# Kernel tuning notes

Hardware: AMD Instinct MI355X
Metric: run time of the kernel (lower is better)

## Reference

```python
import jax, jax.numpy as jnp
import numpy as np

N_NODES = 100000
N_EDGES = 3200000
IN_FEATS = 16
OUT_FEATS = 2
K = 3


def setup_inputs() -> dict:
    key = jax.random.key(0)
    k1, k2, k3, k4 = jax.random.split(key, 4)
    in_feat = jax.random.normal(k1, (N_NODES, IN_FEATS), dtype=jnp.float32)
    # Linear(K*in_feats -> out_feats, bias=False) weight, torch layout (out, in)
    W = jax.random.normal(k2, (OUT_FEATS, K * IN_FEATS), dtype=jnp.float32) * (1.0 / np.sqrt(K * IN_FEATS))
    src = jax.random.randint(k3, (N_EDGES,), 0, N_NODES, dtype=jnp.int64)
    dst = jax.random.randint(k4, (N_EDGES,), 0, N_NODES, dtype=jnp.int64)
    # cached dgl.laplacian_lambda_max value; 2.0 is the normalized-Laplacian bound
    lambda_max = jnp.full((1,), 2.0, dtype=jnp.float32)
    return {"in_feat": in_feat, "W": W, "src": src, "dst": dst, "lambda_max": lambda_max}


def reference(in_feat, W, src, dst, lambda_max):
    N = in_feat.shape[0]
    # in-degree based symmetric normalization, clamp(min=1)
    deg = jax.ops.segment_sum(jnp.ones_like(dst, dtype=in_feat.dtype), dst, num_segments=N)
    norm = jnp.clip(deg, 1.0) ** -0.5  # (N,)
    norm = norm[:, None]
    re_norm = (2.0 / lambda_max)[None, :]  # (1,1), broadcasts over nodes

    def prop(x):
        # D^{-1/2} A D^{-1/2} x via gather from src, scatter-sum to dst
        m = (x * norm)[src]                                    # (E, d)
        return jax.ops.segment_sum(m, dst, num_segments=N) * norm

    X0 = in_feat
    X1 = -re_norm * prop(X0) + X0 * (re_norm - 1.0)
    X2 = -2.0 * re_norm * prop(X1) + X1 * (2.0 * (re_norm - 1.0)) - X0
    Xt = jnp.concatenate([X0, X1, X2], axis=1)                 # (N, K*d)
    h = Xt @ W.T                                               # (N, out)
    return jax.nn.relu(h)  # DGL ChebConv default activation
```

## Files before the change

kernel.cpp:

```cpp
#include <hip/hip_runtime.h>
#include <hip/hip_bf16.h>


#define NN   100000
#define NE   3200000
#define F    16
#define CB   128
#define NBUK 782
#define ECHK 8192
#define NBLK 391
#define LCAP 5632
#define HXW  1025
#define PCAP 4608

__device__ __forceinline__ float bflo(unsigned int u) {
    return __uint_as_float(u << 16);
}
__device__ __forceinline__ float bfhi(unsigned int u) {
    return __uint_as_float(u & 0xffff0000u);
}
__device__ __forceinline__ unsigned int f2bf(float f) {
    __hip_bfloat16 b = __float2bfloat16(f);
    return (unsigned int)*reinterpret_cast<unsigned short*>(&b);
}

__global__ __launch_bounds__(512) void k_lsort(const int* __restrict__ src,
        const int* __restrict__ dst, int* __restrict__ hxg, int* __restrict__ csort) {
    __shared__ __align__(16) int pk[ECHK];
    __shared__ int hx[HXW];
    __shared__ int cur[1024];
    __shared__ int csum[512];
    int t = threadIdx.x, blk = blockIdx.x;
    for (int j = t; j < 1024; j += 512) hx[j] = 0;
    __syncthreads();
    int s0 = blk * ECHK;
    int lim = min(s0 + ECHK, NE);
    int n4 = (lim - s0) >> 2;
    const int4* dst4 = (const int4*)(dst + s0);
    const int4* src4 = (const int4*)(src + s0);
    int4 dreg[4], sreg[4];
#pragma unroll
    for (int k = 0; k < 4; ++k) {
        int i = t + (k << 9);
        if (i < n4) {
            int4 d = dst4[i];
            int4 s = src4[i];
            dreg[k] = d; sreg[k] = s;
            atomicAdd(&hx[d.x >> 7], 1);
            atomicAdd(&hx[d.y >> 7], 1);
            atomicAdd(&hx[d.z >> 7], 1);
            atomicAdd(&hx[d.w >> 7], 1);
        }
    }
    __syncthreads();
    int b0 = t * 2;
    int c0 = hx[b0], c1 = hx[b0 + 1];
    csum[t] = c0 + c1;
    __syncthreads();
    for (int o = 1; o < 512; o <<= 1) {
        int add = (t >= o) ? csum[t - o] : 0;
        __syncthreads();
        csum[t] += add;
        __syncthreads();
    }
    int ce = csum[t] - (c0 + c1);
    hx[b0] = ce;  hx[b0 + 1] = ce + c0;
    cur[b0] = ce; cur[b0 + 1] = ce + c0;
    if (t == 511) hx[1024] = csum[511];
    __syncthreads();
    for (int j = t; j < HXW; j += 512)
        hxg[blk * HXW + j] = hx[j];
#pragma unroll
    for (int k = 0; k < 4; ++k) {
        int i = t + (k << 9);
        if (i < n4) {
            int4 d = dreg[k];
            int4 s = sreg[k];
            int pos;
            pos = atomicAdd(&cur[d.x >> 7], 1); pk[pos] = (s.x << 7) | (d.x & 127);
            pos = atomicAdd(&cur[d.y >> 7], 1); pk[pos] = (s.y << 7) | (d.y & 127);
            pos = atomicAdd(&cur[d.z >> 7], 1); pk[pos] = (s.z << 7) | (d.z & 127);
            pos = atomicAdd(&cur[d.w >> 7], 1); pk[pos] = (s.w << 7) | (d.w & 127);
        }
    }
    __syncthreads();
    int4* cs4 = (int4*)(csort + s0);
    const int4* pk4 = (const int4*)pk;
    for (int i = t; i < n4; i += 512)
        cs4[i] = pk4[i];
}

__global__ __launch_bounds__(512) void k_sort(const int* __restrict__ csort,
        const int* __restrict__ hxg, const float* __restrict__ X0,
        int* __restrict__ es, unsigned int* __restrict__ P,
        unsigned short* __restrict__ Y0, unsigned short* __restrict__ Y1) {
    __shared__ __align__(16) int pk[LCAP];
    __shared__ __align__(16) int pk2[LCAP];
    __shared__ int dsc[512];
    __shared__ int hS[NBLK];
    __shared__ short rls[NBLK];
    __shared__ int wsum[8];
    __shared__ int ws2[2];
    __shared__ int cnt[CB], loc[CB], cur[CB];
    __shared__ float nvs[CB];
    int b = blockIdx.x, t = threadIdx.x;
    int ln = t & 63, wv = t >> 6;
    int h0 = 0, rl = 0;
    if (t < NBLK) {
        h0 = hxg[t * HXW + b];
        rl = hxg[t * HXW + b + 1] - h0;
        hS[t] = h0;
        rls[t] = (short)(rl > 4096 ? 4096 : rl);
    }
    if (t < CB) cnt[t] = 0;
    if (b == 0 && t < 4) {
        ((uint2*)Y0)[(size_t)NN * 4 + t] = make_uint2(0u, 0u);
        ((uint2*)Y1)[(size_t)NN * 4 + t] = make_uint2(0u, 0u);
    }
    int v = rl;
    for (int o = 1; o < 64; o <<= 1) {
        int up = __shfl_up(v, o, 64);
        if (ln >= o) v += up;
    }
    if (ln == 63) wsum[wv] = v;
    __syncthreads();
    if (t == 0) {
        int acc = 0;
        for (int i = 0; i < 8; ++i) { int x = wsum[i]; wsum[i] = acc; acc += x; }
    }
    __syncthreads();
    v += wsum[wv];
    dsc[t] = v;
    __syncthreads();
    int len = dsc[511];
    if (len > LCAP) len = LCAP;
    int g = t >> 4, lane = t & 15;
    for (int c = g; c < NBLK; c += 32) {
        int rlc = rls[c];
        if (rlc == 0) continue;
        int dpos = dsc[c] - rlc;
        if (dpos >= LCAP) continue;
        if (dpos + rlc > LCAP) rlc = LCAP - dpos;
        int sb = c * ECHK + hS[c];
        for (int l = lane; l < rlc; l += 16)
            pk[dpos + l] = csort[sb + l];
    }
    __syncthreads();
    for (int i = t; i < len; i += 512)
        atomicAdd(&cnt[pk[i] & 127], 1);
    __syncthreads();
    int pc = 0, vv = 0;
    if (t < CB) { pc = (cnt[t] + 7) & ~7; vv = pc; }
    for (int o = 1; o < 64; o <<= 1) {
        int up = __shfl_up(vv, o, 64);
        if (ln >= o) vv += up;
    }
    if (t < CB && ln == 63) ws2[wv] = vv;
    __syncthreads();
    if (t < CB) {
        if (wv == 1) vv += ws2[0];
        int excl = vv - pc;
        loc[t] = excl;
        cur[t] = excl;
        int n = b * CB + t;
        if (n < NN) {
            unsigned dgc = cnt[t] > 1023 ? 1023u : (unsigned)cnt[t];
            P[n] = ((unsigned)((b * LCAP + excl) >> 3) << 10) | dgc;
            nvs[t] = rsqrtf((float)(cnt[t] < 1 ? 1 : cnt[t]));
        }
    }
    __syncthreads();
    int plen = loc[CB - 1] + ((cnt[CB - 1] + 7) & ~7);
    if (plen > LCAP) plen = LCAP;
    if (t < CB) {
        int e0 = loc[t] + cnt[t];
        int e1 = loc[t] + ((cnt[t] + 7) & ~7);
        for (int i = e0; i < e1 && i < LCAP; ++i) pk2[i] = NN;
    }
    for (int i = t; i < len; i += 512) {
        int p = pk[i];
        int pos = atomicAdd(&cur[p & 127], 1);
        if (pos < LCAP) pk2[pos] = p >> 7;
    }
    for (int j = t; j < CB * 4; j += 512) {
        int dl = j >> 2;
        int n = b * CB + dl;
        if (n < NN) {
            float nv = nvs[dl];
            size_t g4 = (size_t)n * 4 + (j & 3);
            float4 x0 = ((const float4*)X0)[g4];
            uint2 o;
            o.x = f2bf(x0.x * nv) | (f2bf(x0.y * nv) << 16);
            o.y = f2bf(x0.z * nv) | (f2bf(x0.w * nv) << 16);
            ((uint2*)Y0)[g4] = o;
        }
    }
    __syncthreads();
    int4* es4 = (int4*)(es + b * LCAP);
    const int4* p24 = (const int4*)pk2;
    int p4 = plen >> 2;
    for (int i = t; i < p4; i += 512)
        es4[i] = p24[i];
}

__global__ __launch_bounds__(256) void k_prop1(const unsigned int* __restrict__ P,
        const int* __restrict__ es, const unsigned short* __restrict__ Y0,
        const float* __restrict__ X0, const float* __restrict__ lm,
        unsigned short* __restrict__ Y1) {
    __shared__ __align__(16) int sidx[PCAP];
    int blk = blockIdx.x, t = threadIdx.x;
    int b = blk >> 1, half = blk & 1;
    int n0 = b * CB + half * 64;
    if (n0 >= NN) return;
    unsigned pk0 = P[n0];
    int nL = min(n0 + 63, NN - 1);
    unsigned pkL = P[nL];
    int st = (int)(pk0 >> 10) << 3;
    int en = ((int)(pkL >> 10) << 3) + (int)(((pkL & 1023u) + 7u) & ~7u);
    int slen = en - st;
    if (slen > PCAP) slen = PCAP;
    const int4* esg = (const int4*)(es + st);
    int4* sid4 = (int4*)sidx;
    int s4 = slen >> 2;
    for (int i = t; i < s4; i += 256)
        sid4[i] = esg[i];
    __syncthreads();
    int n = n0 + (t >> 2), h = t & 3;
    if (n >= NN) return;
    unsigned pkn = P[n];
    int beg = ((int)(pkn >> 10) << 3) - st;
    int dg = (int)(pkn & 1023u);
    int nb = (dg + 7) >> 3;
    const uint2* Yv = (const uint2*)Y0;
    float a0 = 0.f, a1 = 0.f, a2 = 0.f, a3 = 0.f;
    for (int bb = 0; bb < nb; ++bb) {
        int e0 = beg + bb * 8;
        int4 ia = *(const int4*)&sidx[e0];
        int4 ib = *(const int4*)&sidx[e0 + 4];
#define ACC(S) { uint2 u = Yv[(size_t)(S) * 4 + h]; \
                 a0 += bflo(u.x); a1 += bfhi(u.x); \
                 a2 += bflo(u.y); a3 += bfhi(u.y); }
        ACC(ia.x) ACC(ia.y) ACC(ia.z) ACC(ia.w)
        ACC(ib.x) ACC(ib.y) ACC(ib.z) ACC(ib.w)
    }
    float nv = rsqrtf((float)(dg < 1 ? 1 : dg));
    float r  = 2.0f / lm[0];
    float k1 = -r * nv, k2 = r - 1.0f;
    int tid4 = n * 4 + h;
    float4 x0 = ((const float4*)X0)[tid4];
    float x1a = k1 * a0 + k2 * x0.x;
    float x1b = k1 * a1 + k2 * x0.y;
    float x1c = k1 * a2 + k2 * x0.z;
    float x1d = k1 * a3 + k2 * x0.w;
    uint2 o;
    o.x = f2bf(nv * x1a) | (f2bf(nv * x1b) << 16);
    o.y = f2bf(nv * x1c) | (f2bf(nv * x1d) << 16);
    ((uint2*)Y1)[tid4] = o;
}

__global__ __launch_bounds__(256) void k_prop2(const unsigned int* __restrict__ P,
        const int* __restrict__ es, const unsigned short* __restrict__ Y1,
        const float* __restrict__ X0, const float* __restrict__ lm,
        const float* __restrict__ W, float* __restrict__ out) {
    __shared__ __align__(16) int sidx[PCAP];
    __shared__ float Ws[96];
    int blk = blockIdx.x, t = threadIdx.x;
    int b = blk >> 1, half = blk & 1;
    int n0 = b * CB + half * 64;
    if (n0 >= NN) return;
    if (t < 96) Ws[t] = W[t];
    unsigned pk0 = P[n0];
    int nL = min(n0 + 63, NN - 1);
    unsigned pkL = P[nL];
    int st = (int)(pk0 >> 10) << 3;
    int en = ((int)(pkL >> 10) << 3) + (int)(((pkL & 1023u) + 7u) & ~7u);
    int slen = en - st;
    if (slen > PCAP) slen = PCAP;
    const int4* esg = (const int4*)(es + st);
    int4* sid4 = (int4*)sidx;
    int s4 = slen >> 2;
    for (int i = t; i < s4; i += 256)
        sid4[i] = esg[i];
    __syncthreads();
    int n = n0 + (t >> 2), h = t & 3;
    if (n >= NN) return;
    unsigned pkn = P[n];
    int beg = ((int)(pkn >> 10) << 3) - st;
    int dg = (int)(pkn & 1023u);
    int nb = (dg + 7) >> 3;
    const uint2* Yv = (const uint2*)Y1;
    float a0 = 0.f, a1 = 0.f, a2 = 0.f, a3 = 0.f;
    for (int bb = 0; bb < nb; ++bb) {
        int e0 = beg + bb * 8;
        int4 ia = *(const int4*)&sidx[e0];
        int4 ib = *(const int4*)&sidx[e0 + 4];
        ACC(ia.x) ACC(ia.y) ACC(ia.z) ACC(ia.w)
        ACC(ib.x) ACC(ib.y) ACC(ib.z) ACC(ib.w)
    }
    int dc = dg < 1 ? 1 : dg;
    float nv = rsqrtf((float)dc);
    float rn = sqrtf((float)dc);
    float r  = 2.0f / lm[0];
    int tid4 = n * 4 + h;
    float4 x0 = ((const float4*)X0)[tid4];
    uint2 uy = ((const uint2*)Y1)[tid4];
    float x1a = bflo(uy.x) * rn, x1b = bfhi(uy.x) * rn;
    float x1c = bflo(uy.y) * rn, x1d = bfhi(uy.y) * rn;
    float c1 = -2.0f * r * nv, c2 = 2.0f * (r - 1.0f);
    float x2a = c1 * a0 + c2 * x1a - x0.x;
    float x2b = c1 * a1 + c2 * x1b - x0.y;
    float x2c = c1 * a2 + c2 * x1c - x0.z;
    float x2d = c1 * a3 + c2 * x1d - x0.w;
    int f0 = 4 * h;
    float t0 = Ws[f0] * x0.x + Ws[f0 + 1] * x0.y + Ws[f0 + 2] * x0.z + Ws[f0 + 3] * x0.w
             + Ws[16 + f0] * x1a + Ws[17 + f0] * x1b + Ws[18 + f0] * x1c + Ws[19 + f0] * x1d
             + Ws[32 + f0] * x2a + Ws[33 + f0] * x2b + Ws[34 + f0] * x2c + Ws[35 + f0] * x2d;
    float t1 = Ws[48 + f0] * x0.x + Ws[49 + f0] * x0.y + Ws[50 + f0] * x0.z + Ws[51 + f0] * x0.w
             + Ws[64 + f0] * x1a + Ws[65 + f0] * x1b + Ws[66 + f0] * x1c + Ws[67 + f0] * x1d
             + Ws[80 + f0] * x2a + Ws[81 + f0] * x2b + Ws[82 + f0] * x2c + Ws[83 + f0] * x2d;
    t0 += __shfl_xor(t0, 2, 4); t0 += __shfl_xor(t0, 1, 4);
    t1 += __shfl_xor(t1, 2, 4); t1 += __shfl_xor(t1, 1, 4);
    if (h == 0) {
        out[(size_t)n * 2 + 0] = fmaxf(t0, 0.f);
        out[(size_t)n * 2 + 1] = fmaxf(t1, 0.f);
    }
}

extern "C" void kernel_launch(void* const* d_in, const int* in_sizes, int n_in,
                              void* d_out, int out_size, void* d_ws, size_t ws_size,
                              hipStream_t stream) {
    const float* X0  = (const float*)d_in[0];
    const float* W   = (const float*)d_in[1];
    const int*   src = (const int*)d_in[2];
    const int*   dst = (const int*)d_in[3];
    const float* lm  = (const float*)d_in[4];
    float* out = (float*)d_out;

    int*   hxg   = (int*)d_ws;
    int*   csort = hxg + (size_t)NBLK * HXW;
    int*   es    = csort + NE;
    unsigned int* P = (unsigned int*)(es + (size_t)NBUK * LCAP);
    unsigned short* Y0 = (unsigned short*)(P + NN);
    unsigned short* Y1 = Y0 + (size_t)(NN + 1) * F;

    k_lsort<<<NBLK, 512, 0, stream>>>(src, dst, hxg, csort);
    k_sort <<<NBUK, 512, 0, stream>>>(csort, hxg, X0, es, P, Y0, Y1);
    k_prop1<<<NBUK * 2, 256, 0, stream>>>(P, es, Y0, X0, lm, Y1);
    k_prop2<<<NBUK * 2, 256, 0, stream>>>(P, es, Y1, X0, lm, W, out);
}
```

Before: 160.4 us.

## Widen gather loads to 16 bytes with lane edge-splitting, use wave-shuffle scan

The gather loops in both propagation kernels now use 16-byte loads covering half a node row: each of the 4 lanes per node takes half the edges and half the features. Partial sums are then combined and redistributed with shuffles. This halves the number of gather load instructions but adds shuffle work and doubles accumulator registers. Separately, the block-wide prefix scan in the local sort replaces a shared-memory Hillis-Steele loop, which had many barriers, with wavefront shuffle scans plus a small per-wave offset pass.

```diff
diff --git a/kernel.cpp b/kernel.cpp
--- a/kernel.cpp
+++ b/kernel.cpp
@@ -29,8 +29,9 @@
     __shared__ __align__(16) int pk[ECHK];
     __shared__ int hx[HXW];
     __shared__ int cur[1024];
-    __shared__ int csum[512];
+    __shared__ int wsum[8];
     int t = threadIdx.x, blk = blockIdx.x;
+    int ln = t & 63, wv = t >> 6;
     for (int j = t; j < 1024; j += 512) hx[j] = 0;
     __syncthreads();
     int s0 = blk * ECHK;
@@ -55,18 +56,23 @@
     __syncthreads();
     int b0 = t * 2;
     int c0 = hx[b0], c1 = hx[b0 + 1];
-    csum[t] = c0 + c1;
-    __syncthreads();
-    for (int o = 1; o < 512; o <<= 1) {
-        int add = (t >= o) ? csum[t - o] : 0;
-        __syncthreads();
-        csum[t] += add;
-        __syncthreads();
-    }
-    int ce = csum[t] - (c0 + c1);
+    int v = c0 + c1;
+    for (int o = 1; o < 64; o <<= 1) {
+        int up = __shfl_up(v, o, 64);
+        if (ln >= o) v += up;
+    }
+    if (ln == 63) wsum[wv] = v;
+    __syncthreads();
+    if (t == 0) {
+        int acc = 0;
+        for (int i = 0; i < 8; ++i) { int x = wsum[i]; wsum[i] = acc; acc += x; }
+    }
+    __syncthreads();
+    v += wsum[wv];
+    int ce = v - (c0 + c1);
     hx[b0] = ce;  hx[b0 + 1] = ce + c0;
     cur[b0] = ce; cur[b0 + 1] = ce + c0;
-    if (t == 511) hx[1024] = csum[511];
+    if (t == 511) hx[1024] = v;
     __syncthreads();
     for (int j = t; j < HXW; j += 512)
         hxg[blk * HXW + j] = hx[j];
@@ -203,14 +209,52 @@
         es4[i] = p24[i];
 }
 
+#define GATHER8(Yv4, half, par, sidx, beg, nb, A)                          \
+    for (int bb = 0; bb < nb; ++bb) {                                      \
+        int e0 = beg + bb * 8;                                             \
+        int4 ia = *(const int4*)&sidx[e0];                                 \
+        int4 ib = *(const int4*)&sidx[e0 + 4];                             \
+        int i0 = par ? ia.y : ia.x;                                        \
+        int i1 = par ? ia.w : ia.z;                                        \
+        int i2 = par ? ib.y : ib.x;                                        \
+        int i3 = par ? ib.w : ib.z;                                        \
+        uint4 u;                                                           \
+        u = Yv4[(size_t)i0 * 2 + half];                                    \
+        A##0 += bflo(u.x); A##1 += bfhi(u.x); A##2 += bflo(u.y); A##3 += bfhi(u.y); \
+        A##4 += bflo(u.z); A##5 += bfhi(u.z); A##6 += bflo(u.w); A##7 += bfhi(u.w); \
+        u = Yv4[(size_t)i1 * 2 + half];                                    \
+        A##0 += bflo(u.x); A##1 += bfhi(u.x); A##2 += bflo(u.y); A##3 += bfhi(u.y); \
+        A##4 += bflo(u.z); A##5 += bfhi(u.z); A##6 += bflo(u.w); A##7 += bfhi(u.w); \
+        u = Yv4[(size_t)i2 * 2 + half];                                    \
+        A##0 += bflo(u.x); A##1 += bfhi(u.x); A##2 += bflo(u.y); A##3 += bfhi(u.y); \
+        A##4 += bflo(u.z); A##5 += bfhi(u.z); A##6 += bflo(u.w); A##7 += bfhi(u.w); \
+        u = Yv4[(size_t)i3 * 2 + half];                                    \
+        A##0 += bflo(u.x); A##1 += bfhi(u.x); A##2 += bflo(u.y); A##3 += bfhi(u.y); \
+        A##4 += bflo(u.z); A##5 += bfhi(u.z); A##6 += bflo(u.w); A##7 += bfhi(u.w); \
+    }
+
+#define REDUCE_REDIST(A, h, r0, r1, r2, r3)                                \
+    A##0 += __shfl_xor(A##0, 2, 4); A##1 += __shfl_xor(A##1, 2, 4);        \
+    A##2 += __shfl_xor(A##2, 2, 4); A##3 += __shfl_xor(A##3, 2, 4);        \
+    A##4 += __shfl_xor(A##4, 2, 4); A##5 += __shfl_xor(A##5, 2, 4);        \
+    A##6 += __shfl_xor(A##6, 2, 4); A##7 += __shfl_xor(A##7, 2, 4);        \
+    {                                                                      \
+        int sl = h >> 1;                                                   \
+        float lo, hi;                                                      \
+        lo = __shfl(A##0, sl, 4); hi = __shfl(A##4, sl, 4); r0 = (h & 1) ? hi : lo; \
+        lo = __shfl(A##1, sl, 4); hi = __shfl(A##5, sl, 4); r1 = (h & 1) ? hi : lo; \
+        lo = __shfl(A##2, sl, 4); hi = __shfl(A##6, sl, 4); r2 = (h & 1) ? hi : lo; \
+        lo = __shfl(A##3, sl, 4); hi = __shfl(A##7, sl, 4); r3 = (h & 1) ? hi : lo; \
+    }
+
 __global__ __launch_bounds__(256) void k_prop1(const unsigned int* __restrict__ P,
         const int* __restrict__ es, const unsigned short* __restrict__ Y0,
         const float* __restrict__ X0, const float* __restrict__ lm,
         unsigned short* __restrict__ Y1) {
     __shared__ __align__(16) int sidx[PCAP];
     int blk = blockIdx.x, t = threadIdx.x;
-    int b = blk >> 1, half = blk & 1;
-    int n0 = b * CB + half * 64;
+    int b = blk >> 1, half_b = blk & 1;
+    int n0 = b * CB + half_b * 64;
     if (n0 >= NN) return;
     unsigned pk0 = P[n0];
     int nL = min(n0 + 63, NN - 1);
@@ -231,27 +275,22 @@
     int beg = ((int)(pkn >> 10) << 3) - st;
     int dg = (int)(pkn & 1023u);
     int nb = (dg + 7) >> 3;
-    const uint2* Yv = (const uint2*)Y0;
-    float a0 = 0.f, a1 = 0.f, a2 = 0.f, a3 = 0.f;
-    for (int bb = 0; bb < nb; ++bb) {
-        int e0 = beg + bb * 8;
-        int4 ia = *(const int4*)&sidx[e0];
-        int4 ib = *(const int4*)&sidx[e0 + 4];
-#define ACC(S) { uint2 u = Yv[(size_t)(S) * 4 + h]; \
-                 a0 += bflo(u.x); a1 += bfhi(u.x); \
-                 a2 += bflo(u.y); a3 += bfhi(u.y); }
-        ACC(ia.x) ACC(ia.y) ACC(ia.z) ACC(ia.w)
-        ACC(ib.x) ACC(ib.y) ACC(ib.z) ACC(ib.w)
-    }
+    const uint4* Yv4 = (const uint4*)Y0;
+    int half = h & 1, par = (h >> 1) & 1;
+    float a0 = 0.f, a1 = 0.f, a2 = 0.f, a3 = 0.f,
+          a4 = 0.f, a5 = 0.f, a6 = 0.f, a7 = 0.f;
+    GATHER8(Yv4, half, par, sidx, beg, nb, a)
+    float r0, r1, r2, r3;
+    REDUCE_REDIST(a, h, r0, r1, r2, r3)
     float nv = rsqrtf((float)(dg < 1 ? 1 : dg));
     float r  = 2.0f / lm[0];
     float k1 = -r * nv, k2 = r - 1.0f;
     int tid4 = n * 4 + h;
     float4 x0 = ((const float4*)X0)[tid4];
-    float x1a = k1 * a0 + k2 * x0.x;
-    float x1b = k1 * a1 + k2 * x0.y;
-    float x1c = k1 * a2 + k2 * x0.z;
-    float x1d = k1 * a3 + k2 * x0.w;
+    float x1a = k1 * r0 + k2 * x0.x;
+    float x1b = k1 * r1 + k2 * x0.y;
+    float x1c = k1 * r2 + k2 * x0.z;
+    float x1d = k1 * r3 + k2 * x0.w;
     uint2 o;
     o.x = f2bf(nv * x1a) | (f2bf(nv * x1b) << 16);
     o.y = f2bf(nv * x1c) | (f2bf(nv * x1d) << 16);
@@ -265,8 +304,8 @@
     __shared__ __align__(16) int sidx[PCAP];
     __shared__ float Ws[96];
     int blk = blockIdx.x, t = threadIdx.x;
-    int b = blk >> 1, half = blk & 1;
-    int n0 = b * CB + half * 64;
+    int b = blk >> 1, half_b = blk & 1;
+    int n0 = b * CB + half_b * 64;
     if (n0 >= NN) return;
     if (t < 96) Ws[t] = W[t];
     unsigned pk0 = P[n0];
@@ -288,15 +327,13 @@
     int beg = ((int)(pkn >> 10) << 3) - st;
     int dg = (int)(pkn & 1023u);
     int nb = (dg + 7) >> 3;
-    const uint2* Yv = (const uint2*)Y1;
-    float a0 = 0.f, a1 = 0.f, a2 = 0.f, a3 = 0.f;
-    for (int bb = 0; bb < nb; ++bb) {
-        int e0 = beg + bb * 8;
-        int4 ia = *(const int4*)&sidx[e0];
-        int4 ib = *(const int4*)&sidx[e0 + 4];
-        ACC(ia.x) ACC(ia.y) ACC(ia.z) ACC(ia.w)
-        ACC(ib.x) ACC(ib.y) ACC(ib.z) ACC(ib.w)
-    }
+    const uint4* Yv4 = (const uint4*)Y1;
+    int half = h & 1, par = (h >> 1) & 1;
+    float a0 = 0.f, a1 = 0.f, a2 = 0.f, a3 = 0.f,
+          a4 = 0.f, a5 = 0.f, a6 = 0.f, a7 = 0.f;
+    GATHER8(Yv4, half, par, sidx, beg, nb, a)
+    float r0, r1, r2, r3;
+    REDUCE_REDIST(a, h, r0, r1, r2, r3)
     int dc = dg < 1 ? 1 : dg;
     float nv = rsqrtf((float)dc);
     float rn = sqrtf((float)dc);
@@ -307,10 +344,10 @@
     float x1a = bflo(uy.x) * rn, x1b = bfhi(uy.x) * rn;
     float x1c = bflo(uy.y) * rn, x1d = bfhi(uy.y) * rn;
     float c1 = -2.0f * r * nv, c2 = 2.0f * (r - 1.0f);
-    float x2a = c1 * a0 + c2 * x1a - x0.x;
-    float x2b = c1 * a1 + c2 * x1b - x0.y;
-    float x2c = c1 * a2 + c2 * x1c - x0.z;
-    float x2d = c1 * a3 + c2 * x1d - x0.w;
+    float x2a = c1 * r0 + c2 * x1a - x0.x;
+    float x2b = c1 * r1 + c2 * x1b - x0.y;
+    float x2c = c1 * r2 + c2 * x1c - x0.z;
+    float x2d = c1 * r3 + c2 * x1d - x0.w;
     int f0 = 4 * h;
     float t0 = Ws[f0] * x0.x + Ws[f0 + 1] * x0.y + Ws[f0 + 2] * x0.z + Ws[f0 + 3] * x0.w
              + Ws[16 + f0] * x1a + Ws[17 + f0] * x1b + Ws[18 + f0] * x1c + Ws[19 + f0] * x1d
```

New measurement: 159.0 us. About the same (-0.9%).
